# Kernel tuning notes

Measured on AMD Instinct MI355X. Metric: run time of the kernel, lower is better.

Reference implementation:

```python
import jax, jax.numpy as jnp
import numpy as np

B, S, HID = 4096, 50, 256
NH = 4
HD = HID // NH          # 64
FB = S // 2 + 1         # 26 freq bins
ALPHA = 0.3
LN_EPS = 1e-12


def setup_inputs() -> dict:
    key = jax.random.key(0)
    ks = jax.random.split(key, 10)
    item = jax.random.normal(ks[0], (B, S, HID), dtype=jnp.float32)
    attr = jax.random.normal(ks[1], (B, S, HID), dtype=jnp.float32)
    complex_weight = jax.random.normal(ks[2], (1, NH, S // 2, HD), dtype=jnp.float32) * 0.02
    base_filter = jnp.ones((NH, FB, 1), dtype=jnp.float32)
    base_bias = jnp.full((NH, FB, 1), -0.1, dtype=jnp.float32)
    # adaptive MLP: Linear(HID,HID) -> GELU -> Linear(HID, NH*FB*2)
    w1 = jax.random.normal(ks[3], (HID, HID), dtype=jnp.float32) * (1.0 / np.sqrt(HID))
    b1 = jnp.zeros((HID,), dtype=jnp.float32)
    w2 = jax.random.normal(ks[4], (HID, NH * FB * 2), dtype=jnp.float32) * (1.0 / np.sqrt(HID))
    b2 = jnp.zeros((NH * FB * 2,), dtype=jnp.float32)
    ln_gamma = jnp.ones((HID,), dtype=jnp.float32)
    ln_beta = jnp.zeros((HID,), dtype=jnp.float32)
    return {
        "item_tensor": item, "attr_tensor": attr,
        "complex_weight": complex_weight,
        "base_filter": base_filter, "base_bias": base_bias,
        "w1": w1, "b1": b1, "w2": w2, "b2": b2,
        "ln_gamma": ln_gamma, "ln_beta": ln_beta,
    }


def _forward(item_tensor, attr_tensor, complex_weight, base_filter, base_bias,
             w1, b1, w2, b2, ln_gamma, ln_beta):
    b, s, hid = item_tensor.shape
    # [B, NH, S, HD]
    x_heads = item_tensor.reshape(b, s, NH, HD).transpose(0, 2, 1, 3)

    # ---- frequency branch ----
    F_fft = jnp.fft.rfft(x_heads, axis=2, norm='ortho')  # [B, NH, FB, HD] complex
    attr_ctx = attr_tensor.mean(axis=1)                   # [B, HID]
    h = jax.nn.gelu(attr_ctx @ w1 + b1, approximate=False)
    adapt = (h @ w2 + b2).reshape(b, NH, FB, 2)
    adaptive_scale = adapt[..., 0:1]
    adaptive_bias = adapt[..., 1:2]
    eff_filter = base_filter * (1.0 + adaptive_scale)     # [B, NH, FB, 1]
    eff_bias = base_bias + adaptive_bias                   # real, added to real part
    F_mod = F_fft * eff_filter + eff_bias
    x_fft = jnp.fft.irfft(F_mod, n=s, axis=2, norm='ortho')  # [B, NH, S, HD]

    # ---- Haar wavelet lifting branch (S even => no truncation/pad) ----
    x_even = x_heads[:, :, 0::2, :]
    x_odd = x_heads[:, :, 1::2, :]
    approx = 0.5 * (x_even + x_odd)
    detail = 0.5 * (x_even - x_odd) * complex_weight
    even_recon = approx + detail
    odd_recon = approx - detail
    # interleave even/odd back: [B, NH, S/2, 2, HD] -> [B, NH, S, HD]
    x_wavelet = jnp.stack([even_recon, odd_recon], axis=3).reshape(b, NH, s, HD)

    # ---- gate combine + residual LayerNorm ----
    x_combined = (1.0 - ALPHA) * x_wavelet + ALPHA * x_fft
    x_out = x_combined.transpose(0, 2, 1, 3).reshape(b, s, hid)
    res = x_out + item_tensor  # dropout is identity in eval
    mu = res.mean(axis=-1, keepdims=True)
    var = jnp.mean(jnp.square(res - mu), axis=-1, keepdims=True)
    return (res - mu) * jax.lax.rsqrt(var + LN_EPS) * ln_gamma + ln_beta


def reference(item_tensor, attr_tensor, complex_weight, base_filter, base_bias,
              w1, b1, w2, b2, ln_gamma, ln_beta):
    return _forward(item_tensor, attr_tensor, complex_weight, base_filter, base_bias,
                    w1, b1, w2, b2, ln_gamma, ln_beta)
```

## Files before the change

### kernel.cpp

```cpp
#include <hip/hip_runtime.h>
#include <math.h>
#include <utility>

#define B_    4096
#define S_    50
#define HID_  256
#define NH_   4
#define HD_   64
#define FB_   26
#define NPAIR 25

__device__ __forceinline__ float rfl_f(float v) {
    union { float f; int i; } u;
    u.f = v;
    u.i = __builtin_amdgcn_readfirstlane(u.i);
    return u.f;
}

__global__ void precompute_kernel(const float* __restrict__ base_filter,
                                  const float* __restrict__ base_bias,
                                  const float* __restrict__ w2,
                                  const float* __restrict__ b2,
                                  float* __restrict__ Wp,
                                  float* __restrict__ C0)
{
    const int m   = blockIdx.x;
    const int j   = threadIdx.x;
    const int h   = m / 100;
    const int rem = m % 100;
    const int cls = rem / 50;
    const int tau = rem % 50;

    const float inv50  = 0.3f / 50.0f;
    const float invs50 = 0.3f * 0.141421356237309515f;

    float acc   = 0.0f;
    float c0acc = 0.0f;
    for (int k = 0; k < FB_; ++k) {
        int   mm   = (k * tau) % 50;
        float cosv = cospif((float)(2 * mm) / 50.0f);
        float wk   = (k == 0 || k == 25) ? 1.0f : 2.0f;
        int   o    = (h * FB_ + k) * 2 + cls;
        float coef;
        if (cls == 0) coef = wk * inv50 * cosv * base_filter[h * FB_ + k];
        else          coef = wk * invs50 * cosv;
        acc += coef * w2[j * 208 + o];
        if (j == 0) {
            if (cls == 0) c0acc += coef * (1.0f + b2[o]);
            else          c0acc += coef * (base_bias[h * FB_ + k] + b2[o]);
        }
    }
    Wp[j * 400 + m] = acc;
    if (j == 0) C0[m] = c0acc;
}

__global__ __launch_bounds__(256)
void mean_kernel(const float* __restrict__ attr, float* __restrict__ ctx)
{
    const int g    = threadIdx.x >> 6;
    const int lane = threadIdx.x & 63;
    const int b    = blockIdx.x * 4 + g;
    const float4* p = (const float4*)(attr + (size_t)b * S_ * HID_) + lane;
    float4 s = make_float4(0.f, 0.f, 0.f, 0.f);
    #pragma unroll
    for (int t = 0; t < S_; ++t) {
        float4 v = p[t * 64];
        s.x += v.x; s.y += v.y; s.z += v.z; s.w += v.w;
    }
    const float is = 1.0f / S_;
    s.x *= is; s.y *= is; s.z *= is; s.w *= is;
    ((float4*)(ctx + (size_t)b * HID_))[lane] = s;
}

template <int EPI>
__global__ __launch_bounds__(256)
void gemm_kernel(const float* __restrict__ A, const float* __restrict__ Bm,
                 const float* __restrict__ bias, float* __restrict__ C,
                 int M, int N, int K)
{
    __shared__ float As[32][36];
    __shared__ float Bs[32][36];
    const int tid = threadIdx.x;
    const int tx = tid & 15, ty = tid >> 4;
    const int col0 = blockIdx.x * 32;
    const int row0 = blockIdx.y * 32;
    const int lr = tid >> 3;
    const int lc = (tid & 7) * 4;

    float acc[2][2] = {};

    for (int k0 = 0; k0 < K; k0 += 32) {
        float4 av = *(const float4*)(A + (size_t)(row0 + lr) * K + k0 + lc);
        *(float4*)&As[lr][lc] = av;
        float4 bv = make_float4(0.f, 0.f, 0.f, 0.f);
        if (col0 + lc + 4 <= N)
            bv = *(const float4*)(Bm + (size_t)(k0 + lr) * N + col0 + lc);
        *(float4*)&Bs[lr][lc] = bv;
        __syncthreads();
        #pragma unroll
        for (int kk = 0; kk < 32; ++kk) {
            float a0 = As[ty * 2][kk],     a1 = As[ty * 2 + 1][kk];
            float b0 = Bs[kk][tx * 2],     b1 = Bs[kk][tx * 2 + 1];
            acc[0][0] = fmaf(a0, b0, acc[0][0]);
            acc[0][1] = fmaf(a0, b1, acc[0][1]);
            acc[1][0] = fmaf(a1, b0, acc[1][0]);
            acc[1][1] = fmaf(a1, b1, acc[1][1]);
        }
        __syncthreads();
    }

    #pragma unroll
    for (int r = 0; r < 2; ++r) {
        int row = row0 + ty * 2 + r;
        #pragma unroll
        for (int c = 0; c < 2; ++c) {
            int col = col0 + tx * 2 + c;
            if (col < N) {
                float v = acc[r][c] + bias[col];
                if (EPI == 0)
                    v = 0.5f * v * (1.0f + erff(v * 0.70710678118654752f));
                C[(size_t)row * N + col] = v;
            }
        }
    }
}

template <int T, int TP>
__device__ __forceinline__ float cval(const float (&cv)[26]) {
    constexpr int ci = ((T - TP) % 50 + 50) % 50;
    constexpr int dd = (ci > 25) ? (50 - ci) : ci;
    return cv[dd];
}

template <int P, int... T>
__device__ __forceinline__ void convPairT(float (&acc)[50], float e, float o,
                                          const float (&cv)[26],
                                          std::integer_sequence<int, T...>) {
    ((acc[T] = fmaf(cval<T, 2 * P>(cv), e, acc[T])), ...);
    ((acc[T] = fmaf(cval<T, 2 * P + 1>(cv), o, acc[T])), ...);
}

template <int P>
__device__ __forceinline__ void convPair(float (&acc)[50],
                                         const float* __restrict__ xp,
                                         const float* __restrict__ cwp,
                                         const float (&cv)[26]) {
    float e   = xp[(2 * P) * HID_];
    float o   = xp[(2 * P + 1) * HID_];
    float cwv = cwp[P * HD_];
    convPairT<P>(acc, e, o, cv, std::make_integer_sequence<int, 50>{});
    float Pc = fmaf(0.35f, cwv, 1.35f);
    float Qc = fmaf(-0.35f, cwv, 0.35f);
    acc[2 * P]     = fmaf(Pc, e, acc[2 * P]);
    acc[2 * P]     = fmaf(Qc, o, acc[2 * P]);
    acc[2 * P + 1] = fmaf(Qc, e, acc[2 * P + 1]);
    acc[2 * P + 1] = fmaf(Pc, o, acc[2 * P + 1]);
}

template <int... Ps>
__device__ __forceinline__ void convAll(float (&acc)[50],
                                        const float* __restrict__ xp,
                                        const float* __restrict__ cwp,
                                        const float (&cv)[26],
                                        std::integer_sequence<int, Ps...>) {
    (convPair<Ps>(acc, xp, cwp, cv), ...);
}

template <int R0>
__device__ __forceinline__ void lnChunk(float (&acc)[50], float (*buf)[HID_],
                                        float2* sums, float gam, float bet,
                                        float* __restrict__ outp,
                                        int tid, int w, int lane)
{
    #pragma unroll
    for (int j = 0; j < 10; ++j) buf[j][tid] = acc[R0 + j];
    __syncthreads();

    #pragma unroll
    for (int rr = 0; rr < 3; ++rr) {
        const int r = w + rr * 4;
        if (r < 10) {
            float4 v = *(const float4*)&buf[r][lane * 4];
            float s  = (v.x + v.y) + (v.z + v.w);
            float qq = v.x * v.x + v.y * v.y + v.z * v.z + v.w * v.w;
            #pragma unroll
            for (int m = 1; m < 64; m <<= 1) {
                s  += __shfl_xor(s,  m, 64);
                qq += __shfl_xor(qq, m, 64);
            }
            if (lane == 0) {
                float mu  = s * (1.0f / HID_);
                float var = qq * (1.0f / HID_) - mu * mu;
                sums[r] = make_float2(mu, rsqrtf(var + 1e-12f));
            }
        }
    }
    __syncthreads();

    #pragma unroll
    for (int j = 0; j < 10; ++j) {
        float2 ms = sums[j];
        outp[(R0 + j) * HID_] = (acc[R0 + j] - ms.x) * ms.y * gam + bet;
    }
}

__global__ __launch_bounds__(256)
__attribute__((amdgpu_waves_per_eu(4)))
void fused_kernel(const float* __restrict__ item,
                  const float* __restrict__ cw,
                  const float* __restrict__ cv,
                  const float* __restrict__ gamma,
                  const float* __restrict__ beta,
                  float* __restrict__ out)
{
    __shared__ float  buf[10][HID_];
    __shared__ float2 sums[10];

    const int b    = blockIdx.x;
    const int tid  = threadIdx.x;
    const int w    = tid >> 6;
    const int lane = tid & 63;
    const int wu   = __builtin_amdgcn_readfirstlane(w);

    const float* cb = cv + (size_t)b * 400 + wu * 100;
    float cvr[26];
    #pragma unroll
    for (int j = 0; j < 26; ++j) cvr[j] = rfl_f(cb[j]);
    const float* vb = cb + 50;

    float acc[50];
    #pragma unroll
    for (int t = 0; t < 50; ++t) acc[t] = rfl_f(vb[t]);

    const float* xp  = item + (size_t)b * S_ * HID_ + tid;
    const float* cwp = cw + (size_t)(wu * NPAIR) * HD_ + lane;

    convAll(acc, xp, cwp, cvr, std::make_integer_sequence<int, NPAIR>{});

    const float gam = gamma[tid];
    const float bet = beta[tid];
    float* outp = out + (size_t)b * S_ * HID_ + tid;

    lnChunk< 0>(acc, buf, sums, gam, bet, outp, tid, w, lane);
    lnChunk<10>(acc, buf, sums, gam, bet, outp, tid, w, lane);
    lnChunk<20>(acc, buf, sums, gam, bet, outp, tid, w, lane);
    lnChunk<30>(acc, buf, sums, gam, bet, outp, tid, w, lane);
    lnChunk<40>(acc, buf, sums, gam, bet, outp, tid, w, lane);
}

extern "C" void kernel_launch(void* const* d_in, const int* in_sizes, int n_in,
                              void* d_out, int out_size, void* d_ws, size_t ws_size,
                              hipStream_t stream)
{
    (void)in_sizes; (void)n_in; (void)out_size; (void)ws_size;
    const float* item = (const float*)d_in[0];
    const float* attr = (const float*)d_in[1];
    const float* cw   = (const float*)d_in[2];
    const float* bf   = (const float*)d_in[3];
    const float* bb   = (const float*)d_in[4];
    const float* w1   = (const float*)d_in[5];
    const float* b1   = (const float*)d_in[6];
    const float* w2   = (const float*)d_in[7];
    const float* b2   = (const float*)d_in[8];
    const float* g    = (const float*)d_in[9];
    const float* be   = (const float*)d_in[10];
    float* out = (float*)d_out;
    float* ws  = (float*)d_ws;

    float* ctx  = ws;
    float* hbuf = ws + 1048576;
    float* Wp   = ws + 2097152;
    float* C0   = ws + 2199552;
    float* cvb  = ws + 2200064;

    hipLaunchKernelGGL(precompute_kernel, dim3(400), dim3(256), 0, stream,
                       bf, bb, w2, b2, Wp, C0);
    hipLaunchKernelGGL(mean_kernel, dim3(B_ / 4), dim3(256), 0, stream, attr, ctx);
    hipLaunchKernelGGL((gemm_kernel<0>), dim3(8, 128), dim3(256), 0, stream,
                       ctx, w1, b1, hbuf, B_, 256, 256);
    hipLaunchKernelGGL((gemm_kernel<1>), dim3(13, 128), dim3(256), 0, stream,
                       hbuf, Wp, C0, cvb, B_, 400, 256);
    hipLaunchKernelGGL(fused_kernel, dim3(B_), dim3(256), 0, stream,
                       item, cw, cvb, g, be, out);
}
```

Before: 572.2 us.

## Fuse attr mean and both MLP GEMMs into one per-batch-tile kernel

Result: no change. 570.7 us (-0.3%).

```diff
diff --git a/kernel.cpp b/kernel.cpp
--- a/kernel.cpp
+++ b/kernel.cpp
@@ -55,73 +55,86 @@
 }
 
 __global__ __launch_bounds__(256)
-void mean_kernel(const float* __restrict__ attr, float* __restrict__ ctx)
-{
-    const int g    = threadIdx.x >> 6;
-    const int lane = threadIdx.x & 63;
-    const int b    = blockIdx.x * 4 + g;
-    const float4* p = (const float4*)(attr + (size_t)b * S_ * HID_) + lane;
-    float4 s = make_float4(0.f, 0.f, 0.f, 0.f);
-    #pragma unroll
-    for (int t = 0; t < S_; ++t) {
-        float4 v = p[t * 64];
-        s.x += v.x; s.y += v.y; s.z += v.z; s.w += v.w;
-    }
-    const float is = 1.0f / S_;
-    s.x *= is; s.y *= is; s.z *= is; s.w *= is;
-    ((float4*)(ctx + (size_t)b * HID_))[lane] = s;
-}
-
-template <int EPI>
-__global__ __launch_bounds__(256)
-void gemm_kernel(const float* __restrict__ A, const float* __restrict__ Bm,
-                 const float* __restrict__ bias, float* __restrict__ C,
-                 int M, int N, int K)
-{
-    __shared__ float As[32][36];
-    __shared__ float Bs[32][36];
-    const int tid = threadIdx.x;
-    const int tx = tid & 15, ty = tid >> 4;
-    const int col0 = blockIdx.x * 32;
-    const int row0 = blockIdx.y * 32;
-    const int lr = tid >> 3;
-    const int lc = (tid & 7) * 4;
-
-    float acc[2][2] = {};
-
-    for (int k0 = 0; k0 < K; k0 += 32) {
-        float4 av = *(const float4*)(A + (size_t)(row0 + lr) * K + k0 + lc);
-        *(float4*)&As[lr][lc] = av;
-        float4 bv = make_float4(0.f, 0.f, 0.f, 0.f);
-        if (col0 + lc + 4 <= N)
-            bv = *(const float4*)(Bm + (size_t)(k0 + lr) * N + col0 + lc);
-        *(float4*)&Bs[lr][lc] = bv;
-        __syncthreads();
-        #pragma unroll
-        for (int kk = 0; kk < 32; ++kk) {
-            float a0 = As[ty * 2][kk],     a1 = As[ty * 2 + 1][kk];
-            float b0 = Bs[kk][tx * 2],     b1 = Bs[kk][tx * 2 + 1];
-            acc[0][0] = fmaf(a0, b0, acc[0][0]);
-            acc[0][1] = fmaf(a0, b1, acc[0][1]);
-            acc[1][0] = fmaf(a1, b0, acc[1][0]);
-            acc[1][1] = fmaf(a1, b1, acc[1][1]);
-        }
-        __syncthreads();
-    }
-
-    #pragma unroll
-    for (int r = 0; r < 2; ++r) {
-        int row = row0 + ty * 2 + r;
-        #pragma unroll
-        for (int c = 0; c < 2; ++c) {
-            int col = col0 + tx * 2 + c;
-            if (col < N) {
-                float v = acc[r][c] + bias[col];
-                if (EPI == 0)
-                    v = 0.5f * v * (1.0f + erff(v * 0.70710678118654752f));
-                C[(size_t)row * N + col] = v;
-            }
-        }
+void mlp_kernel(const float* __restrict__ attr,
+                const float* __restrict__ w1, const float* __restrict__ b1,
+                const float* __restrict__ Wp, const float* __restrict__ C0,
+                float* __restrict__ cvb)
+{
+    __shared__ float ctxL[8][HID_];
+    __shared__ float hL[8][HID_];
+
+    const int tid  = threadIdx.x;
+    const int w    = tid >> 6;
+    const int lane = tid & 63;
+    const int b0   = blockIdx.x * 8;
+
+    #pragma unroll
+    for (int rr = 0; rr < 2; ++rr) {
+        const int r = w + rr * 4;
+        const float4* p = (const float4*)(attr + (size_t)(b0 + r) * S_ * HID_) + lane;
+        float4 s = make_float4(0.f, 0.f, 0.f, 0.f);
+        #pragma unroll
+        for (int t = 0; t < S_; ++t) {
+            float4 v = p[t * 64];
+            s.x += v.x; s.y += v.y; s.z += v.z; s.w += v.w;
+        }
+        const float is = 1.0f / S_;
+        s.x *= is; s.y *= is; s.z *= is; s.w *= is;
+        *(float4*)&ctxL[r][lane * 4] = s;
+    }
+    __syncthreads();
+
+    float h[8] = {};
+    for (int k0 = 0; k0 < HID_; k0 += 4) {
+        float w1v[4];
+        #pragma unroll
+        for (int i = 0; i < 4; ++i) w1v[i] = w1[(size_t)(k0 + i) * HID_ + tid];
+        #pragma unroll
+        for (int r = 0; r < 8; ++r) {
+            float4 c4 = *(const float4*)&ctxL[r][k0];
+            h[r] = fmaf(c4.x, w1v[0], h[r]);
+            h[r] = fmaf(c4.y, w1v[1], h[r]);
+            h[r] = fmaf(c4.z, w1v[2], h[r]);
+            h[r] = fmaf(c4.w, w1v[3], h[r]);
+        }
+    }
+    const float b1v = b1[tid];
+    #pragma unroll
+    for (int r = 0; r < 8; ++r) {
+        float v = h[r] + b1v;
+        hL[r][tid] = 0.5f * v * (1.0f + erff(v * 0.70710678118654752f));
+    }
+    __syncthreads();
+
+    const int  c1   = tid + 256;
+    const bool has1 = (c1 < 400);
+    float a0[8] = {}, a1[8] = {};
+    for (int k0 = 0; k0 < HID_; k0 += 4) {
+        float wv0[4], wv1[4];
+        #pragma unroll
+        for (int i = 0; i < 4; ++i) {
+            wv0[i] = Wp[(size_t)(k0 + i) * 400 + tid];
+            wv1[i] = has1 ? Wp[(size_t)(k0 + i) * 400 + c1] : 0.f;
+        }
+        #pragma unroll
+        for (int r = 0; r < 8; ++r) {
+            float4 h4 = *(const float4*)&hL[r][k0];
+            a0[r] = fmaf(h4.x, wv0[0], a0[r]);
+            a0[r] = fmaf(h4.y, wv0[1], a0[r]);
+            a0[r] = fmaf(h4.z, wv0[2], a0[r]);
+            a0[r] = fmaf(h4.w, wv0[3], a0[r]);
+            a1[r] = fmaf(h4.x, wv1[0], a1[r]);
+            a1[r] = fmaf(h4.y, wv1[1], a1[r]);
+            a1[r] = fmaf(h4.z, wv1[2], a1[r]);
+            a1[r] = fmaf(h4.w, wv1[3], a1[r]);
+        }
+    }
+    const float c0a = C0[tid];
+    const float c0b = has1 ? C0[c1] : 0.f;
+    #pragma unroll
+    for (int r = 0; r < 8; ++r) {
+        cvb[(size_t)(b0 + r) * 400 + tid] = a0[r] + c0a;
+        if (has1) cvb[(size_t)(b0 + r) * 400 + c1] = a1[r] + c0b;
     }
 }
 
@@ -267,19 +280,14 @@
     float* out = (float*)d_out;
     float* ws  = (float*)d_ws;
 
-    float* ctx  = ws;
-    float* hbuf = ws + 1048576;
-    float* Wp   = ws + 2097152;
-    float* C0   = ws + 2199552;
-    float* cvb  = ws + 2200064;
+    float* Wp  = ws;
+    float* C0  = ws + 102400;
+    float* cvb = ws + 102800;
 
     hipLaunchKernelGGL(precompute_kernel, dim3(400), dim3(256), 0, stream,
                        bf, bb, w2, b2, Wp, C0);
-    hipLaunchKernelGGL(mean_kernel, dim3(B_ / 4), dim3(256), 0, stream, attr, ctx);
-    hipLaunchKernelGGL((gemm_kernel<0>), dim3(8, 128), dim3(256), 0, stream,
-                       ctx, w1, b1, hbuf, B_, 256, 256);
-    hipLaunchKernelGGL((gemm_kernel<1>), dim3(13, 128), dim3(256), 0, stream,
-                       hbuf, Wp, C0, cvb, B_, 400, 256);
+    hipLaunchKernelGGL(mlp_kernel, dim3(B_ / 8), dim3(256), 0, stream,
+                       attr, w1, b1, Wp, C0, cvb);
     hipLaunchKernelGGL(fused_kernel, dim3(B_), dim3(256), 0, stream,
                        item, cw, cvb, g, be, out);
 }
```
